# Kernel optimization log

Measured on AMD Instinct MI355X. Metric: run time of the kernel, lower is better.

Reference implementation:

```python
import jax, jax.numpy as jnp
import numpy as np

BS, L, D, H, DC = 8, 8192, 128, 128, 128
C_CONST = 8.0  # rg-lru temperature constant


def _ln(x):
    # LayerNorm without scale/bias (use_bias=False, use_scale=False)
    m = jnp.mean(x, axis=-1, keepdims=True)
    v = jnp.mean(jnp.square(x - m), axis=-1, keepdims=True)
    return (x - m) * jax.lax.rsqrt(v + 1e-6)


def _affine(c, w, b):
    # Dense(features=1)(c)[:, :, None] -> (bs, 1, 1) broadcast scalar per sequence
    return (c @ w + b)[:, :, None]


def _combine(e1, e2):
    a1, b1 = e1
    a2, b2 = e2
    return (a1 * a2, a2 * b1 + b2)


def _linear_scan(a, b, reverse):
    # h_t = a_t * h_{t-1} + b_t (or h_{t+1} when reverse) along seq axis 1
    _, h = jax.lax.associative_scan(_combine, (a, b), axis=1, reverse=reverse)
    return h


def _forward(x, c, cln1_sw, cln1_sb, cln1_bw, cln1_bb, gate1_w, gate1_b,
             rnn_in_w, rnn_in_b, pos_emb, rnn_wi, rnn_bi, rnn_wr, rnn_br, rnn_a,
             rnn_out_w, rnn_out_b, cln2_sw, cln2_sb, cln2_bw, cln2_bb,
             gate2_w, gate2_b, mlp_w1, mlp_b1, mlp_w2, mlp_b2):
    # --- branch 1: conditioned LN -> bidirectional RG-LRU -> gated residual ---
    h = (1.0 + _affine(c, cln1_sw, cln1_sb)) * _ln(x) + _affine(c, cln1_bw, cln1_bb)
    u = _ln(h) @ rnn_in_w + rnn_in_b + pos_emb[None]          # (bs, L, H)
    gi = jax.nn.sigmoid(u @ rnn_wi + rnn_bi)                   # input gate
    gr = jax.nn.sigmoid(u @ rnn_wr + rnn_br)                   # recurrence gate
    at = jnp.exp(C_CONST * gr * jnp.log(rnn_a))                # a_t = a^(c*r_t)
    bt = jnp.sqrt(1.0 - jnp.square(at)) * (gi * u)
    hf = _linear_scan(at, bt, reverse=False)
    hb = _linear_scan(at, bt, reverse=True)
    r = jnp.concatenate([hf, hb], axis=-1) @ rnn_out_w + rnn_out_b  # (bs, L, D)
    x = x + _affine(c, gate1_w, gate1_b) * r
    # --- branch 2: conditioned LN -> gelu MLP -> gated residual ---
    h = (1.0 + _affine(c, cln2_sw, cln2_sb)) * _ln(x) + _affine(c, cln2_bw, cln2_bb)
    m = jax.nn.gelu(h @ mlp_w1 + mlp_b1) @ mlp_w2 + mlp_b2
    return x + _affine(c, gate2_w, gate2_b) * m


def setup_inputs() -> dict:
    key = jax.random.key(0)
    ks = jax.random.split(key, 30)
    def n(k, shape, s=0.05):
        return (jax.random.normal(k, shape) * s).astype(jnp.float32)
    rnn_a = (0.9 + 0.09 * jax.random.uniform(ks[0], (H,))).astype(jnp.float32)
    return {
        "x": jax.random.normal(ks[1], (BS, L, D), jnp.float32),
        "c": jax.random.normal(ks[2], (BS, DC), jnp.float32),
        "cln1_sw": n(ks[3], (DC, 1)), "cln1_sb": n(ks[4], (1,)),
        "cln1_bw": n(ks[5], (DC, 1)), "cln1_bb": n(ks[6], (1,)),
        "gate1_w": n(ks[7], (DC, 1)), "gate1_b": n(ks[8], (1,)),
        "rnn_in_w": n(ks[9], (D, H), 0.1), "rnn_in_b": n(ks[10], (H,)),
        "pos_emb": n(ks[11], (L, H), 0.02),
        "rnn_wi": n(ks[12], (H, H), 0.1), "rnn_bi": n(ks[13], (H,)),
        "rnn_wr": n(ks[14], (H, H), 0.1), "rnn_br": n(ks[15], (H,)),
        "rnn_a": rnn_a,
        "rnn_out_w": n(ks[16], (2 * H, D), 0.1), "rnn_out_b": n(ks[17], (D,)),
        "cln2_sw": n(ks[18], (DC, 1)), "cln2_sb": n(ks[19], (1,)),
        "cln2_bw": n(ks[20], (DC, 1)), "cln2_bb": n(ks[21], (1,)),
        "gate2_w": n(ks[22], (DC, 1)), "gate2_b": n(ks[23], (1,)),
        "mlp_w1": n(ks[24], (D, 4 * D), 0.1), "mlp_b1": n(ks[25], (4 * D,)),
        "mlp_w2": n(ks[26], (4 * D, D), 0.1), "mlp_b2": n(ks[27], (D,)),
    }


def reference(x, c, cln1_sw, cln1_sb, cln1_bw, cln1_bb, gate1_w, gate1_b,
              rnn_in_w, rnn_in_b, pos_emb, rnn_wi, rnn_bi, rnn_wr, rnn_br, rnn_a,
              rnn_out_w, rnn_out_b, cln2_sw, cln2_sb, cln2_bw, cln2_bb,
              gate2_w, gate2_b, mlp_w1, mlp_b1, mlp_w2, mlp_b2):
    return _forward(x, c, cln1_sw, cln1_sb, cln1_bw, cln1_bb, gate1_w, gate1_b,
                    rnn_in_w, rnn_in_b, pos_emb, rnn_wi, rnn_bi, rnn_wr, rnn_br, rnn_a,
                    rnn_out_w, rnn_out_b, cln2_sw, cln2_sb, cln2_bw, cln2_bb,
                    gate2_w, gate2_b, mlp_w1, mlp_b1, mlp_w2, mlp_b2)
```

## Files before the change

kernel.cpp:

```cpp
#include <hip/hip_runtime.h>
#include <hip/hip_bf16.h>

#define BSZ 8
#define SEQ 8192
#define DIM 128
#define NCH 128
#define CLEN 64

typedef unsigned short u16;
typedef unsigned int u32;
typedef short bf16x8 __attribute__((ext_vector_type(8)));
typedef float f32x4  __attribute__((ext_vector_type(4)));

__device__ __forceinline__ float us2f(u16 w){ union{u32 i;float f;}u; u.i=((u32)w)<<16; return u.f; }
__device__ __forceinline__ u16 f2us(float f){
  __hip_bfloat16 h = __float2bfloat16(f);
  union{ __hip_bfloat16 b; u16 s; }u; u.b=h; return u.s;
}
__device__ __forceinline__ float wred64(float v){
  #pragma unroll
  for (int o=1;o<64;o<<=1) v += __shfl_xor(v,o,64);
  return v;
}
__device__ __forceinline__ float red16(float v){
  v += __shfl_xor(v,1,64); v += __shfl_xor(v,2,64);
  v += __shfl_xor(v,4,64); v += __shfl_xor(v,8,64);
  return v;
}
__device__ __forceinline__ float sigmoidf_(float z){ return 1.f/(1.f+__expf(-z)); }
__device__ __forceinline__ float gelu_tanh(float x){
  float y = 0.7978845608028654f * fmaf(0.044715f*x, x*x, x);
  float e = __expf(2.f*y);
  float th = 1.f - 2.f/(e+1.f);
  return 0.5f*x*(1.f+th);
}
__device__ __forceinline__ void lds_fence(){
  asm volatile("s_waitcnt lgkmcnt(0)" ::: "memory");
  __builtin_amdgcn_sched_barrier(0);
}

__global__ __launch_bounds__(64) void k_aff(
    const float* __restrict__ c,
    const float* w0,const float* w1,const float* w2,const float* w3,const float* w4,const float* w5,
    const float* s0,const float* s1,const float* s2,const float* s3,const float* s4,const float* s5,
    float* __restrict__ aff)
{
  const float* ws[6]={w0,w1,w2,w3,w4,w5};
  const float* bs[6]={s0,s1,s2,s3,s4,s5};
  int l = threadIdx.x;
  for (int b=0;b<BSZ;++b){
    #pragma unroll
    for (int h=0;h<6;++h){
      float v = c[b*128+l]*ws[h][l] + c[b*128+64+l]*ws[h][64+l];
      v = wred64(v);
      if (l==0) aff[b*6+h] = v + bs[h][0];
    }
  }
}

__device__ __forceinline__ void pack_one(const float* __restrict__ W, int N,
                                         u16* __restrict__ out, int fi)
{
  int lane = fi & 63;
  int k2   = (fi >> 6) & 1;
  int cn   = fi >> 7;
  int NB   = N >> 4;
  int n    = cn % NB, c = cn / NB;
  int k0   = c*64 + k2*32 + (lane>>4)*8;
  int col  = n*16 + (lane&15);
  u16* o = out + (size_t)fi*8;
  #pragma unroll
  for (int j=0;j<8;++j) o[j] = f2us(W[(size_t)(k0+j)*N + col]);
}

__global__ __launch_bounds__(256) void k_prep(
    const float* __restrict__ w1, const float* __restrict__ w2, const float* __restrict__ wo,
    const float* __restrict__ win, const float* __restrict__ wi, const float* __restrict__ wr,
    u16* __restrict__ w1t, u16* __restrict__ w2t, u16* __restrict__ wot,
    u16* __restrict__ wint, u16* __restrict__ wit, u16* __restrict__ wrt)
{
  int i = blockIdx.x*256 + threadIdx.x;
  if      (i <  8192) pack_one(w1, 512, w1t, i);
  else if (i < 16384) pack_one(w2, 128, w2t, i-8192);
  else if (i < 20480) pack_one(wo, 128, wot, i-16384);
  else if (i < 22528) pack_one(win,128, wint,i-20480);
  else if (i < 24576) pack_one(wi, 128, wit, i-22528);
  else                pack_one(wr, 128, wrt, i-24576);
}

__global__ __launch_bounds__(256,3) void k_pre(
    const float* __restrict__ xg, const u16* __restrict__ wint, const float* __restrict__ b_in,
    const float* __restrict__ pos, const u16* __restrict__ wit, const float* __restrict__ b_i,
    const u16* __restrict__ wrt, const float* __restrict__ b_r, const float* __restrict__ avec,
    const float* __restrict__ aff,
    u32* __restrict__ abg,
    float* __restrict__ Ag, float* __restrict__ Bfg, float* __restrict__ Bbg)
{
  __shared__ u16 A_l[CLEN*136];
  __shared__ u32 abp[CLEN*DIM];
  const int t  = threadIdx.x;
  const int b  = blockIdx.x >> 7;
  const int ck = blockIdx.x & (NCH-1);
  const size_t base = ((size_t)(b*SEQ + ck*CLEN))*DIM;
  const int lane=t&63, wv=t>>6, col=lane&15, quad=lane>>4;
  const int m0 = wv*16;

  {
    const float s1p = 1.f + aff[b*6+0];
    const int ln = t&63;
    for (int i=0;i<16;++i){
      int r = wv*16 + i;
      float2 v = *(const float2*)(xg + base + (size_t)r*DIM + 2*ln);
      float m  = wred64(v.x+v.y)*(1.f/128.f);
      float d0=v.x-m, d1=v.y-m;
      float var = wred64(d0*d0+d1*d1)*(1.f/128.f);
      float rs = rsqrtf(var + 1e-6f);
      float vz = var*rs*rs;
      float tt2 = s1p*rsqrtf(fmaf(s1p*s1p, vz, 1e-6f));
      float sc = rs*tt2;
      u32 pk = (u32)f2us(d0*sc) | ((u32)f2us(d1*sc)<<16);
      *(u32*)&A_l[r*136 + 2*ln] = pk;
    }
  }
  lds_fence();

  f32x4 uacc[8];
  #pragma unroll
  for (int n=0;n<8;++n) uacc[n]=(f32x4){0.f,0.f,0.f,0.f};
  #pragma unroll
  for (int c=0;c<2;++c){
    #pragma unroll
    for (int k2=0;k2<2;++k2){
      bf16x8 av = *(const bf16x8*)&A_l[(m0+col)*136 + c*64 + k2*32 + quad*8];
      #pragma unroll
      for (int n=0;n<8;++n){
        bf16x8 bv = *(const bf16x8*)&wint[(size_t)(((c*8+n)*2+k2)*64+lane)*8];
        uacc[n] = __builtin_amdgcn_mfma_f32_16x16x32_bf16(av, bv, uacc[n], 0,0,0);
      }
    }
  }
  float u_c[8][4];
  #pragma unroll
  for (int n=0;n<8;++n){
    int nc = n*16 + col;
    float bi = b_in[nc];
    #pragma unroll
    for (int r=0;r<4;++r){
      int row = m0 + quad*4 + r;
      u_c[n][r] = uacc[n][r] + bi + pos[(size_t)(ck*CLEN+row)*DIM + nc];
    }
  }
  #pragma unroll
  for (int n=0;n<8;++n){
    #pragma unroll
    for (int r=0;r<4;++r)
      A_l[(m0+quad*4+r)*136 + n*16+col] = f2us(u_c[n][r]);
  }
  lds_fence();

  f32x4 gacc[8], racc[8];
  #pragma unroll
  for (int n=0;n<8;++n){ gacc[n]=(f32x4){0.f,0.f,0.f,0.f}; racc[n]=(f32x4){0.f,0.f,0.f,0.f}; }
  #pragma unroll
  for (int c=0;c<2;++c){
    #pragma unroll
    for (int k2=0;k2<2;++k2){
      bf16x8 av = *(const bf16x8*)&A_l[(m0+col)*136 + c*64 + k2*32 + quad*8];
      #pragma unroll
      for (int n=0;n<8;++n){
        bf16x8 bgi = *(const bf16x8*)&wit[(size_t)(((c*8+n)*2+k2)*64+lane)*8];
        gacc[n] = __builtin_amdgcn_mfma_f32_16x16x32_bf16(av, bgi, gacc[n], 0,0,0);
        bf16x8 bgr = *(const bf16x8*)&wrt[(size_t)(((c*8+n)*2+k2)*64+lane)*8];
        racc[n] = __builtin_amdgcn_mfma_f32_16x16x32_bf16(av, bgr, racc[n], 0,0,0);
      }
    }
  }

  #pragma unroll
  for (int n=0;n<8;++n){
    int nc = n*16 + col;
    float la = __logf(avec[nc]);
    float br = b_r[nc];
    float bi = b_i[nc];
    #pragma unroll
    for (int r=0;r<4;++r){
      int row = m0 + quad*4 + r;
      float gi = sigmoidf_(gacc[n][r]+bi);
      float g  = sigmoidf_(racc[n][r]+br);
      float a  = __expf(8.f*g*la);
      float bb = sqrtf(fmaxf(1.f-a*a,0.f))*gi*u_c[n][r];
      u32 pk = (u32)f2us(a) | ((u32)f2us(bb)<<16);
      abp[row*DIM+nc] = pk;
      abg[base + (size_t)row*DIM + nc] = pk;
    }
  }
  __syncthreads();

  const int sbase = (b*NCH+ck)*DIM;
  if (t < 128){
    float h=0.f, p=1.f;
    #pragma unroll 4
    for (int tt=0;tt<CLEN;++tt){
      u32 v=abp[tt*DIM+t];
      float a=us2f((u16)v), bb=us2f((u16)(v>>16));
      h=fmaf(a,h,bb); p*=a;
    }
    Ag[sbase+t]=p; Bfg[sbase+t]=h;
  } else {
    int ch=t-128; float h=0.f;
    #pragma unroll 4
    for (int tt=CLEN-1;tt>=0;--tt){
      u32 v=abp[tt*DIM+ch];
      h=fmaf(us2f((u16)v),h,us2f((u16)(v>>16)));
    }
    Bbg[sbase+ch]=h;
  }
}

__global__ __launch_bounds__(128) void k_chunkscan(
    const float* __restrict__ Ag, const float* __restrict__ Bfg, const float* __restrict__ Bbg,
    float* __restrict__ Hf, float* __restrict__ Hb)
{
  const int dir = blockIdx.x >> 3, b = blockIdx.x & 7, ch = threadIdx.x;
  float s = 0.f;
  if (dir==0){
    for (int c=0;c<NCH;++c){ size_t i=((size_t)(b*NCH+c))*DIM+ch; Hf[i]=s; s=fmaf(Ag[i],s,Bfg[i]); }
  } else {
    for (int c=NCH-1;c>=0;--c){ size_t i=((size_t)(b*NCH+c))*DIM+ch; Hb[i]=s; s=fmaf(Ag[i],s,Bbg[i]); }
  }
}

__global__ __launch_bounds__(256,2) void k_scan(
    const u32* __restrict__ abg,
    const float* __restrict__ Hf, const float* __restrict__ Hb,
    const float* __restrict__ xg, const u16* __restrict__ wot, const float* __restrict__ b_out,
    const float* __restrict__ aff, float* __restrict__ outg)
{
  __shared__ u32 ab_l[CLEN*DIM];
  __shared__ u16 hcat[CLEN*264];
  const int t  = threadIdx.x;
  const int b  = blockIdx.x >> 7;
  const int ck = blockIdx.x & (NCH-1);
  const size_t base = ((size_t)(b*SEQ + ck*CLEN))*DIM;

  {
    const uint4* src=(const uint4*)(abg+base);
    for (int i=t;i<2048;i+=256) ((uint4*)ab_l)[i]=src[i];
  }
  __syncthreads();

  const int pbase=(b*NCH+ck)*DIM;
  if (t<128){
    float h=Hf[pbase+t];
    #pragma unroll 4
    for (int tt=0;tt<CLEN;++tt){
      u32 v=ab_l[tt*DIM+t];
      h=fmaf(us2f((u16)v),h,us2f((u16)(v>>16)));
      hcat[tt*264+t]=f2us(h);
    }
  } else {
    int ch=t-128;
    float h=Hb[pbase+ch];
    #pragma unroll 4
    for (int tt=CLEN-1;tt>=0;--tt){
      u32 v=ab_l[tt*DIM+ch];
      h=fmaf(us2f((u16)v),h,us2f((u16)(v>>16)));
      hcat[tt*264+128+ch]=f2us(h);
    }
  }
  __syncthreads();

  const int lane=t&63, wv=t>>6, col=lane&15, quad=lane>>4;
  const int m0 = wv*16;
  f32x4 acc[8];
  #pragma unroll
  for (int n=0;n<8;++n) acc[n]=(f32x4){0.f,0.f,0.f,0.f};
  #pragma unroll
  for (int chk=0; chk<4; ++chk){
    #pragma unroll
    for (int k2=0;k2<2;++k2){
      bf16x8 av = *(const bf16x8*)&hcat[(m0+col)*264 + chk*64 + k2*32 + quad*8];
      #pragma unroll
      for (int n=0;n<8;++n){
        bf16x8 bv = *(const bf16x8*)&wot[(size_t)(((chk*8+n)*2+k2)*64+lane)*8];
        acc[n] = __builtin_amdgcn_mfma_f32_16x16x32_bf16(av, bv, acc[n], 0,0,0);
      }
    }
  }
  const float g1=aff[b*6+2];
  #pragma unroll
  for (int n=0;n<8;++n){
    int nc = n*16 + col;
    float bo = b_out[nc];
    #pragma unroll
    for (int r=0;r<4;++r){
      int row = m0 + quad*4 + r;
      size_t gi = base + (size_t)row*DIM + nc;
      outg[gi] = fmaf(g1, acc[n][r]+bo, xg[gi]);
    }
  }
}

__global__ __launch_bounds__(256,2) void k_mlp(
    const u16* __restrict__ w1t, const float* __restrict__ b1v,
    const u16* __restrict__ w2t, const float* __restrict__ b2v,
    const float* __restrict__ aff, float* __restrict__ outg)
{
  __shared__ u16 smem[CLEN*136 + 4*2*16*136];
  u16* h2l = smem;
  u16* m1t = smem + CLEN*136;
  const int t=threadIdx.x;
  const int b=blockIdx.x>>7;
  const size_t base=(size_t)blockIdx.x*CLEN*DIM;
  const int lane=t&63, wv=t>>6, col=lane&15, quad=lane>>4;
  const float s2p=1.f+aff[b*6+3], b2a=aff[b*6+4], g2=aff[b*6+5];
  u16* mw = m1t + wv*(2*16*136);

  {
    const int cg=t&15, rg=t>>4, j0=cg*8, r0=rg*4;
    #pragma unroll
    for (int ii=0;ii<4;++ii){
      int r=r0+ii;
      const float* xo = outg + base + (size_t)r*DIM + j0;
      float4 a = *(const float4*)xo;
      float4 bq = *(const float4*)(xo+4);
      float o[8]={a.x,a.y,a.z,a.w,bq.x,bq.y,bq.z,bq.w};
      float s=0.f;
      #pragma unroll
      for (int j=0;j<8;++j) s+=o[j];
      s=red16(s); float m=s*(1.f/128.f);
      float q2=0.f;
      #pragma unroll
      for (int j=0;j<8;++j){ float d=o[j]-m; q2+=d*d; }
      q2=red16(q2); float rs=rsqrtf(q2*(1.f/128.f)+1e-6f);
      u32 pk[4];
      #pragma unroll
      for (int q=0;q<4;++q){
        float a0=fmaf((o[2*q]-m)*rs,   s2p, b2a);
        float a1=fmaf((o[2*q+1]-m)*rs, s2p, b2a);
        pk[q]= (u32)f2us(a0) | ((u32)f2us(a1)<<16);
      }
      *(uint4*)&h2l[r*136+j0] = make_uint4(pk[0],pk[1],pk[2],pk[3]);
    }
  }
  __syncthreads();

  f32x4 acc2[4][8];
  #pragma unroll
  for (int m=0;m<4;++m)
    #pragma unroll
    for (int n=0;n<8;++n) acc2[m][n]=(f32x4){0.f,0.f,0.f,0.f};

  #pragma unroll
  for (int mp=0;mp<2;++mp){
    #pragma unroll
    for (int h=0;h<2;++h){
      f32x4 a1[2][4];
      #pragma unroll
      for (int m=0;m<2;++m)
        #pragma unroll
        for (int n=0;n<4;++n) a1[m][n]=(f32x4){0.f,0.f,0.f,0.f};
      #pragma unroll
      for (int c=0;c<2;++c){
        #pragma unroll
        for (int k2=0;k2<2;++k2){
          bf16x8 av0 = *(const bf16x8*)&h2l[((2*mp+0)*16+col)*136 + c*64 + k2*32 + quad*8];
          bf16x8 av1 = *(const bf16x8*)&h2l[((2*mp+1)*16+col)*136 + c*64 + k2*32 + quad*8];
          #pragma unroll
          for (int n=0;n<4;++n){
            int ng = wv*8 + h*4 + n;
            bf16x8 bv = *(const bf16x8*)&w1t[(size_t)(((c*32+ng)*2+k2)*64+lane)*8];
            a1[0][n] = __builtin_amdgcn_mfma_f32_16x16x32_bf16(av0, bv, a1[0][n], 0,0,0);
            a1[1][n] = __builtin_amdgcn_mfma_f32_16x16x32_bf16(av1, bv, a1[1][n], 0,0,0);
          }
        }
      }
      lds_fence();
      #pragma unroll
      for (int m=0;m<2;++m){
        #pragma unroll
        for (int n=0;n<4;++n){
          int lc = (h*4+n)*16 + col;
          float bb = b1v[wv*128 + lc];
          #pragma unroll
          for (int r=0;r<4;++r)
            mw[m*(16*136) + (quad*4+r)*136 + lc] = f2us(gelu_tanh(a1[m][n][r] + bb));
        }
      }
    }
    lds_fence();
    #pragma unroll
    for (int c2=0;c2<2;++c2){
      #pragma unroll
      for (int k2=0;k2<2;++k2){
        bf16x8 av0 = *(const bf16x8*)&mw[0*(16*136) + col*136 + c2*64 + k2*32 + quad*8];
        bf16x8 av1 = *(const bf16x8*)&mw[1*(16*136) + col*136 + c2*64 + k2*32 + quad*8];
        int cg = wv*2 + c2;
        #pragma unroll
        for (int n=0;n<8;++n){
          bf16x8 bv = *(const bf16x8*)&w2t[(size_t)(((cg*8+n)*2+k2)*64+lane)*8];
          acc2[2*mp+0][n] = __builtin_amdgcn_mfma_f32_16x16x32_bf16(av0, bv, acc2[2*mp+0][n], 0,0,0);
          acc2[2*mp+1][n] = __builtin_amdgcn_mfma_f32_16x16x32_bf16(av1, bv, acc2[2*mp+1][n], 0,0,0);
        }
      }
    }
  }
  __syncthreads();

  float* pbuf = (float*)smem;
  const int lrow = (lane>>4);
  const int cb   = (lane&15)*8;
  #pragma unroll
  for (int rt=0;rt<4;++rt){
    if (rt) __syncthreads();
    #pragma unroll
    for (int n=0;n<8;++n){
      #pragma unroll
      for (int r=0;r<4;++r)
        pbuf[wv*2048 + (quad*4+r)*128 + n*16+col] = acc2[rt][n][r];
    }
    __syncthreads();
    float s[8] = {0.f,0.f,0.f,0.f,0.f,0.f,0.f,0.f};
    #pragma unroll
    for (int p=0;p<4;++p){
      float4 x0 = *(const float4*)&pbuf[p*2048 + (4*wv+lrow)*128 + cb];
      float4 x1 = *(const float4*)&pbuf[p*2048 + (4*wv+lrow)*128 + cb + 4];
      s[0]+=x0.x; s[1]+=x0.y; s[2]+=x0.z; s[3]+=x0.w;
      s[4]+=x1.x; s[5]+=x1.y; s[6]+=x1.z; s[7]+=x1.w;
    }
    int grow = rt*16 + 4*wv + lrow;
    size_t gi = base + (size_t)grow*DIM + cb;
    float4 o0 = *(const float4*)&outg[gi];
    float4 o1 = *(const float4*)&outg[gi+4];
    float4 bb0 = *(const float4*)&b2v[cb];
    float4 bb1 = *(const float4*)&b2v[cb+4];
    float4 r0, r1;
    r0.x = fmaf(g2, s[0]+bb0.x, o0.x); r0.y = fmaf(g2, s[1]+bb0.y, o0.y);
    r0.z = fmaf(g2, s[2]+bb0.z, o0.z); r0.w = fmaf(g2, s[3]+bb0.w, o0.w);
    r1.x = fmaf(g2, s[4]+bb1.x, o1.x); r1.y = fmaf(g2, s[5]+bb1.y, o1.y);
    r1.z = fmaf(g2, s[6]+bb1.z, o1.z); r1.w = fmaf(g2, s[7]+bb1.w, o1.w);
    *(float4*)&outg[gi]   = r0;
    *(float4*)&outg[gi+4] = r1;
  }
}

extern "C" void kernel_launch(void* const* d_in, const int* in_sizes, int n_in,
                              void* d_out, int out_size, void* d_ws, size_t ws_size,
                              hipStream_t stream)
{
  (void)in_sizes; (void)n_in; (void)out_size; (void)ws_size;
  const float* x   =(const float*)d_in[0];
  const float* c   =(const float*)d_in[1];
  const float* c1sw=(const float*)d_in[2];  const float* c1sb=(const float*)d_in[3];
  const float* c1bw=(const float*)d_in[4];  const float* c1bb=(const float*)d_in[5];
  const float* g1w =(const float*)d_in[6];  const float* g1b =(const float*)d_in[7];
  const float* win =(const float*)d_in[8];  const float* binv=(const float*)d_in[9];
  const float* pos =(const float*)d_in[10];
  const float* wi  =(const float*)d_in[11]; const float* biv =(const float*)d_in[12];
  const float* wr  =(const float*)d_in[13]; const float* brv =(const float*)d_in[14];
  const float* av  =(const float*)d_in[15];
  const float* wout=(const float*)d_in[16]; const float* bout=(const float*)d_in[17];
  const float* c2sw=(const float*)d_in[18]; const float* c2sb=(const float*)d_in[19];
  const float* c2bw=(const float*)d_in[20]; const float* c2bb=(const float*)d_in[21];
  const float* g2w =(const float*)d_in[22]; const float* g2b =(const float*)d_in[23];
  const float* w1  =(const float*)d_in[24]; const float* b1v =(const float*)d_in[25];
  const float* w2  =(const float*)d_in[26]; const float* b2v =(const float*)d_in[27];

  float* wsf  = (float*)d_ws;
  float* Ag   = wsf;
  float* Bfg  = Ag   + 131072;
  float* Bbg  = Bfg  + 131072;
  float* Hf   = Bbg  + 131072;
  float* Hb   = Hf   + 131072;
  float* aff  = Hb   + 131072;
  u16*   w1t  = (u16*)(aff + 64);
  u16*   w2t  = w1t + 65536;
  u16*   wot  = w2t + 65536;
  u16*   wint = wot + 32768;
  u16*   wit  = wint + 16384;
  u16*   wrt  = wit  + 16384;
  u32*   abg  = (u32*)(wrt + 16384);

  float* outg = (float*)d_out;

  k_aff<<<dim3(1),dim3(64),0,stream>>>(c, c1sw,c1bw,g1w,c2sw,c2bw,g2w,
                                       c1sb,c1bb,g1b,c2sb,c2bb,g2b, aff);
  k_prep<<<dim3(104),dim3(256),0,stream>>>(w1,w2,wout,win,wi,wr,
                                           w1t,w2t,wot,wint,wit,wrt);
  k_pre<<<dim3(BSZ*NCH),dim3(256),0,stream>>>(x,wint,binv,pos,wit,biv,wrt,brv,av,aff,
                                              abg, Ag,Bfg,Bbg);
  k_chunkscan<<<dim3(16),dim3(128),0,stream>>>(Ag,Bfg,Bbg,Hf,Hb);
  k_scan<<<dim3(BSZ*NCH),dim3(256),0,stream>>>(abg,Hf,Hb,x,wot,bout,aff,outg);
  k_mlp<<<dim3(BSZ*NCH),dim3(256),0,stream>>>(w1t,b1v,w2t,b2v,aff,outg);
}
```

Measured before the change: 308.9 us.

## Restructure scan kernels: LDS aliasing, parallel chunk scan, coalesced stores and prefetching

k_pre now aliases its LayerNorm staging buffer with the packed a/b buffer to cut LDS use and allow higher occupancy. It also computes LayerNorm with 16-lane groups and vectorized loads, and writes abg with coalesced uint4 copies from LDS. k_chunkscan splits the sequential 128-chunk carry scan into 8 segments per block, composed through shared memory. k_scan drops the LDS staging of abg and instead software-prefetches four steps ahead from global memory. It also stages the output-projection results in LDS so the residual epilogue uses coalesced float4 accesses. The costs are extra barriers and heavier register pressure under the raised launch bounds.

```diff
diff --git a/kernel.cpp b/kernel.cpp
--- a/kernel.cpp
+++ b/kernel.cpp
@@ -88,7 +88,7 @@
   else                pack_one(wr, 128, wrt, i-24576);
 }
 
-__global__ __launch_bounds__(256,3) void k_pre(
+__global__ __launch_bounds__(256,4) void k_pre(
     const float* __restrict__ xg, const u16* __restrict__ wint, const float* __restrict__ b_in,
     const float* __restrict__ pos, const u16* __restrict__ wit, const float* __restrict__ b_i,
     const u16* __restrict__ wrt, const float* __restrict__ b_r, const float* __restrict__ avec,
@@ -96,8 +96,8 @@
     u32* __restrict__ abg,
     float* __restrict__ Ag, float* __restrict__ Bfg, float* __restrict__ Bbg)
 {
-  __shared__ u16 A_l[CLEN*136];
-  __shared__ u32 abp[CLEN*DIM];
+  __shared__ __align__(16) u32 abp[CLEN*DIM];
+  u16* A_l = (u16*)abp;
   const int t  = threadIdx.x;
   const int b  = blockIdx.x >> 7;
   const int ck = blockIdx.x & (NCH-1);
@@ -107,19 +107,32 @@
 
   {
     const float s1p = 1.f + aff[b*6+0];
-    const int ln = t&63;
-    for (int i=0;i<16;++i){
-      int r = wv*16 + i;
-      float2 v = *(const float2*)(xg + base + (size_t)r*DIM + 2*ln);
-      float m  = wred64(v.x+v.y)*(1.f/128.f);
-      float d0=v.x-m, d1=v.y-m;
-      float var = wred64(d0*d0+d1*d1)*(1.f/128.f);
-      float rs = rsqrtf(var + 1e-6f);
-      float vz = var*rs*rs;
-      float tt2 = s1p*rsqrtf(fmaf(s1p*s1p, vz, 1e-6f));
-      float sc = rs*tt2;
-      u32 pk = (u32)f2us(d0*sc) | ((u32)f2us(d1*sc)<<16);
-      *(u32*)&A_l[r*136 + 2*ln] = pk;
+    const int cg=t&15, rg=t>>4, j0=cg*8, r0=rg*4;
+    #pragma unroll
+    for (int ii=0;ii<4;++ii){
+      int r=r0+ii;
+      const float* xo = xg + base + (size_t)r*DIM + j0;
+      float4 a = *(const float4*)xo;
+      float4 bq = *(const float4*)(xo+4);
+      float o[8]={a.x,a.y,a.z,a.w,bq.x,bq.y,bq.z,bq.w};
+      float s=0.f;
+      #pragma unroll
+      for (int j=0;j<8;++j) s+=o[j];
+      s=red16(s); float m=s*(1.f/128.f);
+      float q2=0.f;
+      #pragma unroll
+      for (int j=0;j<8;++j){ float d=o[j]-m; q2+=d*d; }
+      q2=red16(q2); float var=q2*(1.f/128.f);
+      float rs=rsqrtf(var+1e-6f);
+      float vz=var*rs*rs;
+      float tt2=s1p*rsqrtf(fmaf(s1p*s1p,vz,1e-6f));
+      float sc=rs*tt2;
+      u32 pk[4];
+      #pragma unroll
+      for (int q=0;q<4;++q){
+        pk[q]= (u32)f2us((o[2*q]-m)*sc) | ((u32)f2us((o[2*q+1]-m)*sc)<<16);
+      }
+      *(uint4*)&A_l[r*136+j0] = make_uint4(pk[0],pk[1],pk[2],pk[3]);
     }
   }
   lds_fence();
@@ -175,6 +188,7 @@
       }
     }
   }
+  __syncthreads();
 
   #pragma unroll
   for (int n=0;n<8;++n){
@@ -189,12 +203,17 @@
       float g  = sigmoidf_(racc[n][r]+br);
       float a  = __expf(8.f*g*la);
       float bb = sqrtf(fmaxf(1.f-a*a,0.f))*gi*u_c[n][r];
-      u32 pk = (u32)f2us(a) | ((u32)f2us(bb)<<16);
-      abp[row*DIM+nc] = pk;
-      abg[base + (size_t)row*DIM + nc] = pk;
-    }
-  }
-  __syncthreads();
+      abp[row*DIM+nc] = (u32)f2us(a) | ((u32)f2us(bb)<<16);
+    }
+  }
+  __syncthreads();
+
+  {
+    uint4* dst = (uint4*)(abg + base);
+    const uint4* src = (const uint4*)abp;
+    #pragma unroll
+    for (int i=t;i<2048;i+=256) dst[i]=src[i];
+  }
 
   const int sbase = (b*NCH+ck)*DIM;
   if (t < 128){
@@ -217,55 +236,95 @@
   }
 }
 
-__global__ __launch_bounds__(128) void k_chunkscan(
+__global__ __launch_bounds__(1024) void k_chunkscan(
     const float* __restrict__ Ag, const float* __restrict__ Bfg, const float* __restrict__ Bbg,
     float* __restrict__ Hf, float* __restrict__ Hb)
 {
-  const int dir = blockIdx.x >> 3, b = blockIdx.x & 7, ch = threadIdx.x;
-  float s = 0.f;
+  __shared__ float sP[8][128], sS[8][128];
+  const int dir = blockIdx.x >> 3, b = blockIdx.x & 7;
+  const int t = threadIdx.x, seg = t>>7, ch = t&127;
+  const size_t cbase = (size_t)b*NCH*DIM + ch;
+  float P=1.f, S=0.f;
   if (dir==0){
-    for (int c=0;c<NCH;++c){ size_t i=((size_t)(b*NCH+c))*DIM+ch; Hf[i]=s; s=fmaf(Ag[i],s,Bfg[i]); }
+    #pragma unroll 4
+    for (int j=0;j<16;++j){
+      size_t i = cbase + (size_t)(seg*16+j)*DIM;
+      float a=Ag[i]; S=fmaf(a,S,Bfg[i]); P*=a;
+    }
   } else {
-    for (int c=NCH-1;c>=0;--c){ size_t i=((size_t)(b*NCH+c))*DIM+ch; Hb[i]=s; s=fmaf(Ag[i],s,Bbg[i]); }
-  }
-}
-
-__global__ __launch_bounds__(256,2) void k_scan(
+    #pragma unroll 4
+    for (int j=15;j>=0;--j){
+      size_t i = cbase + (size_t)(seg*16+j)*DIM;
+      float a=Ag[i]; S=fmaf(a,S,Bbg[i]); P*=a;
+    }
+  }
+  sP[seg][ch]=P; sS[seg][ch]=S;
+  __syncthreads();
+  float h=0.f;
+  if (dir==0){ for (int s=0;s<seg;++s) h=fmaf(sP[s][ch],h,sS[s][ch]); }
+  else       { for (int s=7;s>seg;--s) h=fmaf(sP[s][ch],h,sS[s][ch]); }
+  if (dir==0){
+    #pragma unroll 4
+    for (int j=0;j<16;++j){
+      size_t i = cbase + (size_t)(seg*16+j)*DIM;
+      Hf[i]=h; h=fmaf(Ag[i],h,Bfg[i]);
+    }
+  } else {
+    #pragma unroll 4
+    for (int j=15;j>=0;--j){
+      size_t i = cbase + (size_t)(seg*16+j)*DIM;
+      Hb[i]=h; h=fmaf(Ag[i],h,Bbg[i]);
+    }
+  }
+}
+
+__global__ __launch_bounds__(256,4) void k_scan(
     const u32* __restrict__ abg,
     const float* __restrict__ Hf, const float* __restrict__ Hb,
     const float* __restrict__ xg, const u16* __restrict__ wot, const float* __restrict__ b_out,
     const float* __restrict__ aff, float* __restrict__ outg)
 {
-  __shared__ u32 ab_l[CLEN*DIM];
-  __shared__ u16 hcat[CLEN*264];
+  __shared__ __align__(16) u16 hcat[CLEN*264];
   const int t  = threadIdx.x;
   const int b  = blockIdx.x >> 7;
   const int ck = blockIdx.x & (NCH-1);
   const size_t base = ((size_t)(b*SEQ + ck*CLEN))*DIM;
-
-  {
-    const uint4* src=(const uint4*)(abg+base);
-    for (int i=t;i<2048;i+=256) ((uint4*)ab_l)[i]=src[i];
-  }
-  __syncthreads();
-
   const int pbase=(b*NCH+ck)*DIM;
+
   if (t<128){
-    float h=Hf[pbase+t];
-    #pragma unroll 4
-    for (int tt=0;tt<CLEN;++tt){
-      u32 v=ab_l[tt*DIM+t];
-      h=fmaf(us2f((u16)v),h,us2f((u16)(v>>16)));
-      hcat[tt*264+t]=f2us(h);
+    const u32* p = abg + base + t;
+    float h = Hf[pbase+t];
+    u32 v0=p[0], v1=p[128], v2=p[256], v3=p[384];
+    #pragma unroll
+    for (int g=0; g<16; ++g){
+      u32 n0=0,n1=0,n2=0,n3=0;
+      if (g<15){
+        n0=p[(g*4+4)*128]; n1=p[(g*4+5)*128];
+        n2=p[(g*4+6)*128]; n3=p[(g*4+7)*128];
+      }
+      h=fmaf(us2f((u16)v0),h,us2f((u16)(v0>>16))); hcat[(g*4+0)*264+t]=f2us(h);
+      h=fmaf(us2f((u16)v1),h,us2f((u16)(v1>>16))); hcat[(g*4+1)*264+t]=f2us(h);
+      h=fmaf(us2f((u16)v2),h,us2f((u16)(v2>>16))); hcat[(g*4+2)*264+t]=f2us(h);
+      h=fmaf(us2f((u16)v3),h,us2f((u16)(v3>>16))); hcat[(g*4+3)*264+t]=f2us(h);
+      v0=n0; v1=n1; v2=n2; v3=n3;
     }
   } else {
     int ch=t-128;
-    float h=Hb[pbase+ch];
-    #pragma unroll 4
-    for (int tt=CLEN-1;tt>=0;--tt){
-      u32 v=ab_l[tt*DIM+ch];
-      h=fmaf(us2f((u16)v),h,us2f((u16)(v>>16)));
-      hcat[tt*264+128+ch]=f2us(h);
+    const u32* p = abg + base + ch;
+    float h = Hb[pbase+ch];
+    u32 v0=p[63*128], v1=p[62*128], v2=p[61*128], v3=p[60*128];
+    #pragma unroll
+    for (int g=0; g<16; ++g){
+      u32 n0=0,n1=0,n2=0,n3=0;
+      if (g<15){
+        n0=p[(59-g*4)*128]; n1=p[(58-g*4)*128];
+        n2=p[(57-g*4)*128]; n3=p[(56-g*4)*128];
+      }
+      h=fmaf(us2f((u16)v0),h,us2f((u16)(v0>>16))); hcat[(63-g*4)*264+128+ch]=f2us(h);
+      h=fmaf(us2f((u16)v1),h,us2f((u16)(v1>>16))); hcat[(62-g*4)*264+128+ch]=f2us(h);
+      h=fmaf(us2f((u16)v2),h,us2f((u16)(v2>>16))); hcat[(61-g*4)*264+128+ch]=f2us(h);
+      h=fmaf(us2f((u16)v3),h,us2f((u16)(v3>>16))); hcat[(60-g*4)*264+128+ch]=f2us(h);
+      v0=n0; v1=n1; v2=n2; v3=n3;
     }
   }
   __syncthreads();
@@ -287,17 +346,29 @@
       }
     }
   }
+  __syncthreads();
+  float* pbuf = (float*)hcat;
+  #pragma unroll
+  for (int n=0;n<8;++n){
+    #pragma unroll
+    for (int r=0;r<4;++r)
+      pbuf[(m0+quad*4+r)*128 + n*16+col] = acc[n][r];
+  }
+  __syncthreads();
+
   const float g1=aff[b*6+2];
-  #pragma unroll
-  for (int n=0;n<8;++n){
-    int nc = n*16 + col;
-    float bo = b_out[nc];
-    #pragma unroll
-    for (int r=0;r<4;++r){
-      int row = m0 + quad*4 + r;
-      size_t gi = base + (size_t)row*DIM + nc;
-      outg[gi] = fmaf(g1, acc[n][r]+bo, xg[gi]);
-    }
+  const float4* xv4 = (const float4*)(xg+base);
+  float4* ov4 = (float4*)(outg+base);
+  const float4* cv4 = (const float4*)pbuf;
+  #pragma unroll
+  for (int i=t;i<2048;i+=256){
+    float4 cv = cv4[i];
+    float4 xv = xv4[i];
+    float4 bo = *(const float4*)&b_out[(i*4)&127];
+    float4 r;
+    r.x=fmaf(g1,cv.x+bo.x,xv.x); r.y=fmaf(g1,cv.y+bo.y,xv.y);
+    r.z=fmaf(g1,cv.z+bo.z,xv.z); r.w=fmaf(g1,cv.w+bo.w,xv.w);
+    ov4[i]=r;
   }
 }
 
@@ -489,7 +560,7 @@
                                            w1t,w2t,wot,wint,wit,wrt);
   k_pre<<<dim3(BSZ*NCH),dim3(256),0,stream>>>(x,wint,binv,pos,wit,biv,wrt,brv,av,aff,
                                               abg, Ag,Bfg,Bbg);
-  k_chunkscan<<<dim3(16),dim3(128),0,stream>>>(Ag,Bfg,Bbg,Hf,Hb);
+  k_chunkscan<<<dim3(16),dim3(1024),0,stream>>>(Ag,Bfg,Bbg,Hf,Hb);
   k_scan<<<dim3(BSZ*NCH),dim3(256),0,stream>>>(abg,Hf,Hb,x,wot,bout,aff,outg);
   k_mlp<<<dim3(BSZ*NCH),dim3(256),0,stream>>>(w1t,b1v,w2t,b2v,aff,outg);
 }
```

After: 271.1 us. -12.3%, faster.
